# Performance work log

Measured on AMD Instinct MI355X. Metric: run time of the kernel, lower is better.

The kernel has to match this reference:

```python
import jax, jax.numpy as jnp
import numpy as np

N_NODES = 200000
N_EDGES = 800000
C1, E1 = 20000, 80000
C2, E2 = 2000, 8000
N_IN, N_HID, K_BLOCK = 24, 64, 6
N_OUT = 6
BN_EPS = 1e-5


def cheb_conv(x, edge_index, W, b, n):
    """PyG ChebConv with lambda_max=2: L_hat = -D^-1/2 A D^-1/2."""
    src, dst = edge_index[0], edge_index[1]
    K = W.shape[0]
    deg = jax.ops.segment_sum(jnp.ones(src.shape[0], x.dtype), dst, num_segments=n)
    dis = jnp.where(deg > 0, 1.0 / jnp.sqrt(jnp.maximum(deg, 1.0)), 0.0)
    norm = -(dis[src] * dis[dst])[:, None]  # [E,1]

    def prop(h):
        return jax.ops.segment_sum(h[src] * norm, dst, num_segments=n)

    Tx0 = x
    out = Tx0 @ W[0]
    if K > 1:
        Tx1 = prop(Tx0)
        out = out + Tx1 @ W[1]
        for k in range(2, K):
            Tx2 = 2.0 * prop(Tx1) - Tx0
            out = out + Tx2 @ W[k]
            Tx0, Tx1 = Tx1, Tx2
    return out + b


def batchnorm(h, g, bt):
    m = jnp.mean(h, axis=0)
    v = jnp.mean((h - m) ** 2, axis=0)  # biased var, as torch BN forward
    return (h - m) / jnp.sqrt(v + BN_EPS) * g + bt


def kipf_block(x, edge_index, W, b, g, bt, n):
    return jax.nn.relu(batchnorm(cheb_conv(x, edge_index, W, b, n), g, bt))


def segment_mean(x, seg, n_seg):
    s = jax.ops.segment_sum(x, seg, num_segments=n_seg)
    cnt = jax.ops.segment_sum(jnp.ones(x.shape[0], x.dtype), seg, num_segments=n_seg)
    return s / jnp.maximum(cnt, 1.0)[:, None]


def setup_inputs() -> dict:
    key = jax.random.key(0)
    ks = jax.random.split(key, 12)
    inp = {
        "x": jax.random.normal(ks[0], (N_NODES, N_IN), jnp.float32),
        "edge_index": jax.random.randint(ks[1], (2, N_EDGES), 0, N_NODES),
        "cluster1": jax.random.randint(ks[2], (N_NODES,), 0, C1),
        "cluster2": jax.random.randint(ks[3], (N_NODES,), 0, C2),
        "edge_index_c1": jax.random.randint(ks[4], (2, E1), 0, C1),
        "edge_index_c2": jax.random.randint(ks[5], (2, E2), 0, C2),
    }
    sc = 1.0 / np.sqrt(N_IN * K_BLOCK)
    for i, kk in zip((1, 2, 3), (ks[6], ks[7], ks[8])):
        inp[f"W{i}"] = jax.random.normal(kk, (K_BLOCK, N_IN, N_HID), jnp.float32) * sc
        inp[f"b{i}"] = jnp.zeros((N_HID,), jnp.float32)
        inp[f"g{i}"] = jnp.ones((N_HID,), jnp.float32)
        inp[f"bt{i}"] = jnp.zeros((N_HID,), jnp.float32)
    n_mix = 3 * N_HID + N_IN
    inp["Wm"] = jax.random.normal(ks[9], (1, n_mix, N_OUT), jnp.float32) / np.sqrt(n_mix)
    inp["bm"] = jnp.zeros((N_OUT,), jnp.float32)
    return inp


def reference(x, edge_index, cluster1, cluster2, edge_index_c1, edge_index_c2,
              W1, b1, g1, bt1, W2, b2, g2, bt2, W3, b3, g3, bt3, Wm, bm):
    # branch 1: full-resolution graph
    h1 = kipf_block(x, edge_index, W1, b1, g1, bt1, N_NODES)
    # branch 2: cluster1-pooled graph, then unpool
    xp1 = segment_mean(x, cluster1, C1)
    h2 = kipf_block(xp1, edge_index_c1, W2, b2, g2, bt2, C1)[cluster1]
    # branch 3: cluster2-pooled graph, then unpool
    xp2 = segment_mean(x, cluster2, C2)
    h3 = kipf_block(xp2, edge_index_c2, W3, b3, g3, bt3, C2)[cluster2]
    # skip concat with raw input, then mixing conv (K=1 -> identity Cheb term)
    mix = jnp.concatenate([h1, h2, h3, x], axis=1)
    return cheb_conv(mix, edge_index, Wm, bm, N_NODES)
```

## Files before the change

kernel.cpp:

```cpp
#include <hip/hip_runtime.h>
#include <algorithm>

#define FIN 24
#define NHID 64
#define NMIX 216
#define NOUT 6
#define BN_EPS 1e-5f

__global__ void k_hist(const int* __restrict__ ei, int E, int* deg) {
    int e = blockIdx.x * blockDim.x + threadIdx.x;
    if (e < E) atomicAdd(&deg[ei[E + e]], 1);
}

__global__ void k_dis(const int* __restrict__ deg, float* dis, int n) {
    int i = blockIdx.x * blockDim.x + threadIdx.x;
    if (i < n) { int v = deg[i]; dis[i] = v > 0 ? rsqrtf((float)v) : 0.f; }
}

__global__ void k_scan_local(const int* __restrict__ deg, int n, int* rowptr, int* bsum) {
    __shared__ int s[256];
    int i = blockIdx.x * 256 + threadIdx.x;
    int v = (i < n) ? deg[i] : 0;
    s[threadIdx.x] = v;
    __syncthreads();
#pragma unroll
    for (int off = 1; off < 256; off <<= 1) {
        int x = (threadIdx.x >= off) ? s[threadIdx.x - off] : 0;
        __syncthreads();
        s[threadIdx.x] += x;
        __syncthreads();
    }
    if (i <= n) rowptr[i] = s[threadIdx.x] - v;
    if (threadIdx.x == 255) bsum[blockIdx.x] = s[255];
}

__global__ void k_scan_bsum(int* bsum, int nb) {
    __shared__ int s[256];
    int carry = 0;
    for (int base = 0; base < nb; base += 256) {
        int i = base + threadIdx.x;
        int v = (i < nb) ? bsum[i] : 0;
        s[threadIdx.x] = v;
        __syncthreads();
#pragma unroll
        for (int off = 1; off < 256; off <<= 1) {
            int x = (threadIdx.x >= off) ? s[threadIdx.x - off] : 0;
            __syncthreads();
            s[threadIdx.x] += x;
            __syncthreads();
        }
        if (i < nb) bsum[i] = s[threadIdx.x] - v + carry;
        carry += s[255];
        __syncthreads();
    }
}

__global__ void k_scan_add(int* rowptr, const int* __restrict__ bsum, int n) {
    int i = blockIdx.x * 256 + threadIdx.x;
    if (i <= n) rowptr[i] += bsum[blockIdx.x];
}

__global__ void k_fill(const int* __restrict__ ei, int E, const float* __restrict__ dis,
                       const int* __restrict__ rowptr, int* fill,
                       int* __restrict__ col, float* __restrict__ val) {
    int e = blockIdx.x * blockDim.x + threadIdx.x;
    if (e >= E) return;
    int s = ei[e], d = ei[E + e];
    int slot = rowptr[d] + atomicAdd(&fill[d], 1);
    col[slot] = s;
    val[slot] = -dis[s] * dis[d];
}

__global__ void k_propg(const int* __restrict__ rowptr, const int* __restrict__ col,
                        const float* __restrict__ val, float scale,
                        const float* __restrict__ h, const float* __restrict__ prev,
                        float* __restrict__ out, int n) {
    int t = blockIdx.x * blockDim.x + threadIdx.x;
    if (t >= n) return;
    int beg = rowptr[t], end = rowptr[t + 1];
    float4 a[6];
#pragma unroll
    for (int q = 0; q < 6; ++q) a[q] = make_float4(0.f, 0.f, 0.f, 0.f);
    for (int e = beg; e < end; ++e) {
        float w = val[e];
        const float4* hp = reinterpret_cast<const float4*>(h + (size_t)col[e] * FIN);
#pragma unroll
        for (int q = 0; q < 6; ++q) {
            float4 hv = hp[q];
            a[q].x = fmaf(w, hv.x, a[q].x);
            a[q].y = fmaf(w, hv.y, a[q].y);
            a[q].z = fmaf(w, hv.z, a[q].z);
            a[q].w = fmaf(w, hv.w, a[q].w);
        }
    }
    float4* op = reinterpret_cast<float4*>(out + (size_t)t * FIN);
    if (prev) {
        const float4* pp = reinterpret_cast<const float4*>(prev + (size_t)t * FIN);
#pragma unroll
        for (int q = 0; q < 6; ++q) {
            float4 pv = pp[q];
            op[q] = make_float4(fmaf(scale, a[q].x, -pv.x), fmaf(scale, a[q].y, -pv.y),
                                fmaf(scale, a[q].z, -pv.z), fmaf(scale, a[q].w, -pv.w));
        }
    } else {
#pragma unroll
        for (int q = 0; q < 6; ++q)
            op[q] = make_float4(scale * a[q].x, scale * a[q].y, scale * a[q].z, scale * a[q].w);
    }
}

__global__ void k_gemv2(const float* __restrict__ S1, const float* __restrict__ S2,
                        const float* __restrict__ Wa, const float* __restrict__ Wb,
                        const float* __restrict__ bias, float* __restrict__ acc,
                        float* __restrict__ stats, int n) {
    __shared__ float sb[4][2][16 * FIN];
    int j = threadIdx.x & 63;
    int w = threadIdx.x >> 6;
    float wa[FIN], wb[FIN];
#pragma unroll
    for (int f = 0; f < FIN; ++f) wa[f] = Wa[f * NHID + j];
#pragma unroll
    for (int f = 0; f < FIN; ++f) wb[f] = Wb[f * NHID + j];
    int nbase = blockIdx.x * 64 + w * 16;
#pragma unroll
    for (int k = 0; k < 3; ++k) {
        int i = k * 64 + j;
        int half = i / 96;
        int j4 = i - half * 96;
        int nd = j4 / 6, q = j4 - nd * 6;
        int node = nbase + nd;
        const float* src = (half ? S2 : S1) + (size_t)node * FIN + q * 4;
        float4 v = (node < n) ? *reinterpret_cast<const float4*>(src)
                              : make_float4(0.f, 0.f, 0.f, 0.f);
        *reinterpret_cast<float4*>(&sb[w][half][j4 * 4]) = v;
    }
    float sum = 0.f, sq = 0.f;
#pragma unroll 2
    for (int nd = 0; nd < 16; ++nd) {
        int node = nbase + nd;
        bool ok = (node < n);
        int nodec = ok ? node : 0;
        float base = bias ? bias[j] : acc[(size_t)nodec * NHID + j];
        const float4* r1 = reinterpret_cast<const float4*>(&sb[w][0][nd * FIN]);
        const float4* r2 = reinterpret_cast<const float4*>(&sb[w][1][nd * FIN]);
        float a = 0.f, p = 0.f;
#pragma unroll
        for (int t = 0; t < 6; ++t) {
            float4 v = r1[t];
            a = fmaf(v.x, wa[t * 4 + 0], a);
            p = fmaf(v.y, wa[t * 4 + 1], p);
            a = fmaf(v.z, wa[t * 4 + 2], a);
            p = fmaf(v.w, wa[t * 4 + 3], p);
        }
#pragma unroll
        for (int t = 0; t < 6; ++t) {
            float4 v = r2[t];
            a = fmaf(v.x, wb[t * 4 + 0], a);
            p = fmaf(v.y, wb[t * 4 + 1], p);
            a = fmaf(v.z, wb[t * 4 + 2], a);
            p = fmaf(v.w, wb[t * 4 + 3], p);
        }
        float r = base + a + p;
        if (ok) {
            acc[(size_t)node * NHID + j] = r;
            sum += r; sq = fmaf(r, r, sq);
        }
    }
    if (stats) {
        __shared__ float rs[256], rq[256];
        rs[threadIdx.x] = sum; rq[threadIdx.x] = sq;
        __syncthreads();
        if (threadIdx.x < 64) {
            float s = rs[threadIdx.x] + rs[threadIdx.x + 64] + rs[threadIdx.x + 128] + rs[threadIdx.x + 192];
            float q = rq[threadIdx.x] + rq[threadIdx.x + 64] + rq[threadIdx.x + 128] + rq[threadIdx.x + 192];
            atomicAdd(&stats[threadIdx.x], s);
            atomicAdd(&stats[NHID + threadIdx.x], q);
        }
    }
}

__global__ void k_bnprep3(const float* __restrict__ st1, const float* __restrict__ g1,
                          const float* __restrict__ bt1, float inv1,
                          const float* __restrict__ st2, const float* __restrict__ g2,
                          const float* __restrict__ bt2, float inv2,
                          const float* __restrict__ st3, const float* __restrict__ g3,
                          const float* __restrict__ bt3, float inv3,
                          float* __restrict__ s1, float* __restrict__ s2,
                          float* __restrict__ s3) {
    int b = threadIdx.x >> 6, i = threadIdx.x & 63;
    const float* st = (b == 0) ? st1 : (b == 1) ? st2 : st3;
    const float* g  = (b == 0) ? g1  : (b == 1) ? g2  : g3;
    const float* bt = (b == 0) ? bt1 : (b == 1) ? bt2 : bt3;
    float inv       = (b == 0) ? inv1 : (b == 1) ? inv2 : inv3;
    float* so       = (b == 0) ? s1  : (b == 1) ? s2  : s3;
    float m = st[i] * inv;
    float v = st[NHID + i] * inv - m * m;
    float sc = g[i] * rsqrtf(v + BN_EPS);
    so[i] = sc;
    so[NHID + i] = fmaf(-m, sc, bt[i]);
}

__global__ void k_scatter(const float* __restrict__ x, const int* __restrict__ cl,
                          int n, float* xp, float* cnt) {
    int idx = blockIdx.x * blockDim.x + threadIdx.x;
    if (idx >= n * FIN) return;
    int node = idx / FIN, f = idx - node * FIN;
    int c = cl[node];
    atomicAdd(&xp[c * FIN + f], x[idx]);
    if (f == 0) atomicAdd(&cnt[c], 1.f);
}

__global__ void k_divcnt(float* xp, const float* __restrict__ cnt, int c) {
    int idx = blockIdx.x * blockDim.x + threadIdx.x;
    if (idx >= c * FIN) return;
    xp[idx] = xp[idx] / fmaxf(cnt[idx / FIN], 1.f);
}

__global__ void k_final(const float* __restrict__ acc1, const float* __restrict__ sc1,
                        const float* __restrict__ h2, const float* __restrict__ sc2,
                        const int* __restrict__ cl1,
                        const float* __restrict__ h3, const float* __restrict__ sc3,
                        const int* __restrict__ cl2,
                        const float* __restrict__ x, const float* __restrict__ Wm,
                        const float* __restrict__ bm, float* __restrict__ out, int n) {
    int t = blockIdx.x * blockDim.x + threadIdx.x;
    if (t >= n) return;
    float o[NOUT];
#pragma unroll
    for (int j = 0; j < NOUT; ++j) o[j] = bm[j];
    {
        const float4* r4 = reinterpret_cast<const float4*>(acc1 + (size_t)t * NHID);
#pragma unroll
        for (int i4 = 0; i4 < NHID / 4; ++i4) {
            float4 v = r4[i4];
            float hv[4] = {v.x, v.y, v.z, v.w};
#pragma unroll
            for (int c = 0; c < 4; ++c) {
                int i = i4 * 4 + c;
                float h = fmaxf(fmaf(hv[c], sc1[i], sc1[NHID + i]), 0.f);
#pragma unroll
                for (int j = 0; j < NOUT; ++j) o[j] = fmaf(h, Wm[i * NOUT + j], o[j]);
            }
        }
    }
    {
        const float4* r4 = reinterpret_cast<const float4*>(h2 + (size_t)cl1[t] * NHID);
#pragma unroll
        for (int i4 = 0; i4 < NHID / 4; ++i4) {
            float4 v = r4[i4];
            float hv[4] = {v.x, v.y, v.z, v.w};
#pragma unroll
            for (int c = 0; c < 4; ++c) {
                int hid = i4 * 4 + c;
                float h = fmaxf(fmaf(hv[c], sc2[hid], sc2[NHID + hid]), 0.f);
#pragma unroll
                for (int j = 0; j < NOUT; ++j) o[j] = fmaf(h, Wm[(NHID + hid) * NOUT + j], o[j]);
            }
        }
    }
    {
        const float4* r4 = reinterpret_cast<const float4*>(h3 + (size_t)cl2[t] * NHID);
#pragma unroll
        for (int i4 = 0; i4 < NHID / 4; ++i4) {
            float4 v = r4[i4];
            float hv[4] = {v.x, v.y, v.z, v.w};
#pragma unroll
            for (int c = 0; c < 4; ++c) {
                int hid = i4 * 4 + c;
                float h = fmaxf(fmaf(hv[c], sc3[hid], sc3[NHID + hid]), 0.f);
#pragma unroll
                for (int j = 0; j < NOUT; ++j) o[j] = fmaf(h, Wm[(2 * NHID + hid) * NOUT + j], o[j]);
            }
        }
    }
    {
        const float4* r4 = reinterpret_cast<const float4*>(x + (size_t)t * FIN);
#pragma unroll
        for (int i4 = 0; i4 < FIN / 4; ++i4) {
            float4 v = r4[i4];
            float hv[4] = {v.x, v.y, v.z, v.w};
#pragma unroll
            for (int c = 0; c < 4; ++c) {
                int i = 3 * NHID + i4 * 4 + c;
#pragma unroll
                for (int j = 0; j < NOUT; ++j) o[j] = fmaf(hv[c], Wm[i * NOUT + j], o[j]);
            }
        }
    }
    float* op = out + (size_t)t * NOUT;
#pragma unroll
    for (int j = 0; j < NOUT; ++j) op[j] = o[j];
}

extern "C" void kernel_launch(void* const* d_in, const int* in_sizes, int n_in,
                              void* d_out, int out_size, void* d_ws, size_t ws_size,
                              hipStream_t stream) {
    const int N = 200000, E = 800000;
    const int C1n = 20000, E1 = 80000;
    const int C2n = 2000, E2 = 8000;

    const float* x  = (const float*)d_in[0];
    const int* ei   = (const int*)d_in[1];
    const int* cl1  = (const int*)d_in[2];
    const int* cl2  = (const int*)d_in[3];
    const int* eic1 = (const int*)d_in[4];
    const int* eic2 = (const int*)d_in[5];
    const float* W1 = (const float*)d_in[6];  const float* b1 = (const float*)d_in[7];
    const float* g1 = (const float*)d_in[8];  const float* bt1 = (const float*)d_in[9];
    const float* W2 = (const float*)d_in[10]; const float* b2 = (const float*)d_in[11];
    const float* g2 = (const float*)d_in[12]; const float* bt2 = (const float*)d_in[13];
    const float* W3 = (const float*)d_in[14]; const float* b3 = (const float*)d_in[15];
    const float* g3 = (const float*)d_in[16]; const float* bt3 = (const float*)d_in[17];
    const float* Wm = (const float*)d_in[18]; const float* bm = (const float*)d_in[19];

    char* wb = (char*)d_ws;
    size_t off = 0;
    auto alloc = [&](size_t nwords) {
        void* p = wb + off; off += ((nwords + 3) & ~(size_t)3) * 4; return p;
    };
    int* degi1 = (int*)alloc(N);   int* fill1 = (int*)alloc(N);
    int* degi2 = (int*)alloc(C1n); int* fill2 = (int*)alloc(C1n);
    int* degi3 = (int*)alloc(C2n); int* fill3 = (int*)alloc(C2n);
    float* st1 = (float*)alloc(128); float* st2 = (float*)alloc(128); float* st3 = (float*)alloc(128);
    float* xp1 = (float*)alloc((size_t)C1n * FIN); float* cnt1 = (float*)alloc(C1n);
    float* xp2 = (float*)alloc((size_t)C2n * FIN); float* cnt2 = (float*)alloc(C2n);
    size_t zero_bytes = off;
    int* rp1 = (int*)alloc(N + 1);   int* col1 = (int*)alloc(E);  float* val1 = (float*)alloc(E);
    int* rp2 = (int*)alloc(C1n + 1); int* col2 = (int*)alloc(E1); float* val2 = (float*)alloc(E1);
    int* rp3 = (int*)alloc(C2n + 1); int* col3 = (int*)alloc(E2); float* val3 = (float*)alloc(E2);
    float* dis1 = (float*)alloc(N); float* dis2 = (float*)alloc(C1n); float* dis3 = (float*)alloc(C2n);
    int* bsum = (int*)alloc(1024);
    float* scsh1 = (float*)alloc(128); float* scsh2 = (float*)alloc(128); float* scsh3 = (float*)alloc(128);
    float* B1_0 = (float*)alloc((size_t)N * FIN);   float* B1_1 = (float*)alloc((size_t)N * FIN);
    float* B2_0 = (float*)alloc((size_t)C1n * FIN); float* B2_1 = (float*)alloc((size_t)C1n * FIN);
    float* B3_0 = (float*)alloc((size_t)C2n * FIN); float* B3_1 = (float*)alloc((size_t)C2n * FIN);
    float* acc1 = (float*)alloc((size_t)N * NHID);
    float* acc2 = (float*)alloc((size_t)C1n * NHID);
    float* acc3 = (float*)alloc((size_t)C2n * NHID);
    if (off > ws_size) return;

    hipMemsetAsync(d_ws, 0, zero_bytes, stream);

    const int T = 256;
    auto cdiv = [](int a, int b) { return (a + b - 1) / b; };

    auto branch = [&](const float* xin, int n, const int* e, int Ecnt,
                      const float* W, const float* bb, int* degi, int* fill, float* dis,
                      int* rp, int* col, float* val,
                      float* B0, float* Bb1, float* acc, float* st) {
        int ge = cdiv(Ecnt, T), gn = cdiv(n, T);
        int nb = cdiv(n + 1, 256);
        int gg = cdiv(n, 64);
        const int WSZ = FIN * NHID;
        k_hist<<<ge, T, 0, stream>>>(e, Ecnt, degi);
        k_dis<<<gn, T, 0, stream>>>(degi, dis, n);
        k_scan_local<<<nb, 256, 0, stream>>>(degi, n, rp, bsum);
        k_scan_bsum<<<1, 256, 0, stream>>>(bsum, nb);
        k_scan_add<<<nb, 256, 0, stream>>>(rp, bsum, n);
        k_fill<<<ge, T, 0, stream>>>(e, Ecnt, dis, rp, fill, col, val);
        k_propg<<<gn, T, 0, stream>>>(rp, col, val, 1.0f, xin, nullptr, B0, n);
        k_gemv2<<<gg, T, 0, stream>>>(xin, B0, W, W + WSZ, bb, acc, nullptr, n);
        k_propg<<<gn, T, 0, stream>>>(rp, col, val, 2.0f, B0, xin, Bb1, n);
        k_propg<<<gn, T, 0, stream>>>(rp, col, val, 2.0f, Bb1, B0, B0, n);
        k_gemv2<<<gg, T, 0, stream>>>(Bb1, B0, W + 2 * WSZ, W + 3 * WSZ, nullptr, acc, nullptr, n);
        k_propg<<<gn, T, 0, stream>>>(rp, col, val, 2.0f, B0, Bb1, Bb1, n);
        k_propg<<<gn, T, 0, stream>>>(rp, col, val, 2.0f, Bb1, B0, B0, n);
        k_gemv2<<<gg, T, 0, stream>>>(Bb1, B0, W + 4 * WSZ, W + 5 * WSZ, nullptr, acc, st, n);
    };

    branch(x, N, ei, E, W1, b1, degi1, fill1, dis1, rp1, col1, val1, B1_0, B1_1, acc1, st1);
    k_scatter<<<cdiv(N * FIN, T), T, 0, stream>>>(x, cl1, N, xp1, cnt1);
    k_divcnt<<<cdiv(C1n * FIN, T), T, 0, stream>>>(xp1, cnt1, C1n);
    branch(xp1, C1n, eic1, E1, W2, b2, degi2, fill2, dis2, rp2, col2, val2, B2_0, B2_1, acc2, st2);
    k_scatter<<<cdiv(N * FIN, T), T, 0, stream>>>(x, cl2, N, xp2, cnt2);
    k_divcnt<<<cdiv(C2n * FIN, T), T, 0, stream>>>(xp2, cnt2, C2n);
    branch(xp2, C2n, eic2, E2, W3, b3, degi3, fill3, dis3, rp3, col3, val3, B3_0, B3_1, acc3, st3);
    k_bnprep3<<<1, 192, 0, stream>>>(st1, g1, bt1, 1.0f / (float)N,
                                     st2, g2, bt2, 1.0f / (float)C1n,
                                     st3, g3, bt3, 1.0f / (float)C2n,
                                     scsh1, scsh2, scsh3);
    k_final<<<cdiv(N, T), T, 0, stream>>>(acc1, scsh1, acc2, scsh2, cl1,
                                          acc3, scsh3, cl2,
                                          x, Wm, bm, (float*)d_out, N);
}
```

Baseline: 760.8 us.

## Split SpMM propagation across six threads per node and pack CSR col/val

The propagation kernel now assigns one float4 feature chunk per thread, six threads per node, so neighbor-row gathers are coalesced across lanes. Edges are unrolled by two with dual accumulators. The CSR column and weight arrays are packed into one int2 array so each edge needs a single load. The gemv kernel preloads the 16 base values per thread before the loop and fully unrolls it, at the cost of more registers. Each thread now re-reads rowptr and the edge list redundantly, six times per node.

Measured after the change: 679.6 us. 10.7% less time.

```diff
diff --git a/kernel.cpp b/kernel.cpp
--- a/kernel.cpp
+++ b/kernel.cpp
@@ -61,52 +61,52 @@
 }
 
 __global__ void k_fill(const int* __restrict__ ei, int E, const float* __restrict__ dis,
-                       const int* __restrict__ rowptr, int* fill,
-                       int* __restrict__ col, float* __restrict__ val) {
+                       const int* __restrict__ rowptr, int* fill, int2* __restrict__ cv) {
     int e = blockIdx.x * blockDim.x + threadIdx.x;
     if (e >= E) return;
     int s = ei[e], d = ei[E + e];
     int slot = rowptr[d] + atomicAdd(&fill[d], 1);
-    col[slot] = s;
-    val[slot] = -dis[s] * dis[d];
-}
-
-__global__ void k_propg(const int* __restrict__ rowptr, const int* __restrict__ col,
-                        const float* __restrict__ val, float scale,
-                        const float* __restrict__ h, const float* __restrict__ prev,
-                        float* __restrict__ out, int n) {
-    int t = blockIdx.x * blockDim.x + threadIdx.x;
-    if (t >= n) return;
-    int beg = rowptr[t], end = rowptr[t + 1];
-    float4 a[6];
-#pragma unroll
-    for (int q = 0; q < 6; ++q) a[q] = make_float4(0.f, 0.f, 0.f, 0.f);
-    for (int e = beg; e < end; ++e) {
-        float w = val[e];
-        const float4* hp = reinterpret_cast<const float4*>(h + (size_t)col[e] * FIN);
-#pragma unroll
-        for (int q = 0; q < 6; ++q) {
-            float4 hv = hp[q];
-            a[q].x = fmaf(w, hv.x, a[q].x);
-            a[q].y = fmaf(w, hv.y, a[q].y);
-            a[q].z = fmaf(w, hv.z, a[q].z);
-            a[q].w = fmaf(w, hv.w, a[q].w);
-        }
-    }
-    float4* op = reinterpret_cast<float4*>(out + (size_t)t * FIN);
+    cv[slot] = make_int2(s, __float_as_int(-dis[s] * dis[d]));
+}
+
+__global__ void k_propg(const int* __restrict__ rowptr, const int2* __restrict__ cv,
+                        float scale, const float* __restrict__ h,
+                        const float* __restrict__ prev, float* __restrict__ out, int n) {
+    int idx = blockIdx.x * blockDim.x + threadIdx.x;
+    if (idx >= n * 6) return;
+    int d = idx / 6, q = idx - d * 6;
+    int beg = rowptr[d], end = rowptr[d + 1];
+    const float4* h4 = reinterpret_cast<const float4*>(h);
+    float ax = 0.f, ay = 0.f, az = 0.f, aw = 0.f;
+    float bx = 0.f, by = 0.f, bz = 0.f, bw = 0.f;
+    int e = beg;
+    for (; e + 2 <= end; e += 2) {
+        int2 c0 = cv[e], c1 = cv[e + 1];
+        float w0 = __int_as_float(c0.y), w1 = __int_as_float(c1.y);
+        float4 h0 = h4[(size_t)c0.x * 6 + q];
+        float4 h1 = h4[(size_t)c1.x * 6 + q];
+        ax = fmaf(w0, h0.x, ax); ay = fmaf(w0, h0.y, ay);
+        az = fmaf(w0, h0.z, az); aw = fmaf(w0, h0.w, aw);
+        bx = fmaf(w1, h1.x, bx); by = fmaf(w1, h1.y, by);
+        bz = fmaf(w1, h1.z, bz); bw = fmaf(w1, h1.w, bw);
+    }
+    if (e < end) {
+        int2 c0 = cv[e];
+        float w0 = __int_as_float(c0.y);
+        float4 h0 = h4[(size_t)c0.x * 6 + q];
+        ax = fmaf(w0, h0.x, ax); ay = fmaf(w0, h0.y, ay);
+        az = fmaf(w0, h0.z, az); aw = fmaf(w0, h0.w, aw);
+    }
+    ax += bx; ay += by; az += bz; aw += bw;
+    float4 r;
     if (prev) {
-        const float4* pp = reinterpret_cast<const float4*>(prev + (size_t)t * FIN);
-#pragma unroll
-        for (int q = 0; q < 6; ++q) {
-            float4 pv = pp[q];
-            op[q] = make_float4(fmaf(scale, a[q].x, -pv.x), fmaf(scale, a[q].y, -pv.y),
-                                fmaf(scale, a[q].z, -pv.z), fmaf(scale, a[q].w, -pv.w));
-        }
+        float4 pv = reinterpret_cast<const float4*>(prev)[idx];
+        r = make_float4(fmaf(scale, ax, -pv.x), fmaf(scale, ay, -pv.y),
+                        fmaf(scale, az, -pv.z), fmaf(scale, aw, -pv.w));
     } else {
-#pragma unroll
-        for (int q = 0; q < 6; ++q)
-            op[q] = make_float4(scale * a[q].x, scale * a[q].y, scale * a[q].z, scale * a[q].w);
-    }
+        r = make_float4(scale * ax, scale * ay, scale * az, scale * aw);
+    }
+    reinterpret_cast<float4*>(out)[idx] = r;
 }
 
 __global__ void k_gemv2(const float* __restrict__ S1, const float* __restrict__ S2,
@@ -116,12 +116,24 @@
     __shared__ float sb[4][2][16 * FIN];
     int j = threadIdx.x & 63;
     int w = threadIdx.x >> 6;
+    int nbase = blockIdx.x * 64 + w * 16;
+    float bases[16];
+    if (bias) {
+        float bb = bias[j];
+#pragma unroll
+        for (int nd = 0; nd < 16; ++nd) bases[nd] = bb;
+    } else {
+#pragma unroll
+        for (int nd = 0; nd < 16; ++nd) {
+            int node = nbase + nd;
+            bases[nd] = (node < n) ? acc[(size_t)node * NHID + j] : 0.f;
+        }
+    }
     float wa[FIN], wb[FIN];
 #pragma unroll
     for (int f = 0; f < FIN; ++f) wa[f] = Wa[f * NHID + j];
 #pragma unroll
     for (int f = 0; f < FIN; ++f) wb[f] = Wb[f * NHID + j];
-    int nbase = blockIdx.x * 64 + w * 16;
 #pragma unroll
     for (int k = 0; k < 3; ++k) {
         int i = k * 64 + j;
@@ -135,12 +147,9 @@
         *reinterpret_cast<float4*>(&sb[w][half][j4 * 4]) = v;
     }
     float sum = 0.f, sq = 0.f;
-#pragma unroll 2
+#pragma unroll
     for (int nd = 0; nd < 16; ++nd) {
         int node = nbase + nd;
-        bool ok = (node < n);
-        int nodec = ok ? node : 0;
-        float base = bias ? bias[j] : acc[(size_t)nodec * NHID + j];
         const float4* r1 = reinterpret_cast<const float4*>(&sb[w][0][nd * FIN]);
         const float4* r2 = reinterpret_cast<const float4*>(&sb[w][1][nd * FIN]);
         float a = 0.f, p = 0.f;
@@ -160,8 +169,8 @@
             a = fmaf(v.z, wb[t * 4 + 2], a);
             p = fmaf(v.w, wb[t * 4 + 3], p);
         }
-        float r = base + a + p;
-        if (ok) {
+        float r = bases[nd] + a + p;
+        if (node < n) {
             acc[(size_t)node * NHID + j] = r;
             sum += r; sq = fmaf(r, r, sq);
         }
@@ -325,9 +334,9 @@
     float* xp1 = (float*)alloc((size_t)C1n * FIN); float* cnt1 = (float*)alloc(C1n);
     float* xp2 = (float*)alloc((size_t)C2n * FIN); float* cnt2 = (float*)alloc(C2n);
     size_t zero_bytes = off;
-    int* rp1 = (int*)alloc(N + 1);   int* col1 = (int*)alloc(E);  float* val1 = (float*)alloc(E);
-    int* rp2 = (int*)alloc(C1n + 1); int* col2 = (int*)alloc(E1); float* val2 = (float*)alloc(E1);
-    int* rp3 = (int*)alloc(C2n + 1); int* col3 = (int*)alloc(E2); float* val3 = (float*)alloc(E2);
+    int* rp1 = (int*)alloc(N + 1);   int2* cv1 = (int2*)alloc(2 * (size_t)E);
+    int* rp2 = (int*)alloc(C1n + 1); int2* cv2 = (int2*)alloc(2 * (size_t)E1);
+    int* rp3 = (int*)alloc(C2n + 1); int2* cv3 = (int2*)alloc(2 * (size_t)E2);
     float* dis1 = (float*)alloc(N); float* dis2 = (float*)alloc(C1n); float* dis3 = (float*)alloc(C2n);
     int* bsum = (int*)alloc(1024);
     float* scsh1 = (float*)alloc(128); float* scsh2 = (float*)alloc(128); float* scsh3 = (float*)alloc(128);
@@ -346,35 +355,35 @@
 
     auto branch = [&](const float* xin, int n, const int* e, int Ecnt,
                       const float* W, const float* bb, int* degi, int* fill, float* dis,
-                      int* rp, int* col, float* val,
-                      float* B0, float* Bb1, float* acc, float* st) {
+                      int* rp, int2* cv, float* B0, float* Bb1, float* acc, float* st) {
         int ge = cdiv(Ecnt, T), gn = cdiv(n, T);
         int nb = cdiv(n + 1, 256);
         int gg = cdiv(n, 64);
+        int gp = cdiv(n * 6, T);
         const int WSZ = FIN * NHID;
         k_hist<<<ge, T, 0, stream>>>(e, Ecnt, degi);
         k_dis<<<gn, T, 0, stream>>>(degi, dis, n);
         k_scan_local<<<nb, 256, 0, stream>>>(degi, n, rp, bsum);
         k_scan_bsum<<<1, 256, 0, stream>>>(bsum, nb);
         k_scan_add<<<nb, 256, 0, stream>>>(rp, bsum, n);
-        k_fill<<<ge, T, 0, stream>>>(e, Ecnt, dis, rp, fill, col, val);
-        k_propg<<<gn, T, 0, stream>>>(rp, col, val, 1.0f, xin, nullptr, B0, n);
+        k_fill<<<ge, T, 0, stream>>>(e, Ecnt, dis, rp, fill, cv);
+        k_propg<<<gp, T, 0, stream>>>(rp, cv, 1.0f, xin, nullptr, B0, n);
         k_gemv2<<<gg, T, 0, stream>>>(xin, B0, W, W + WSZ, bb, acc, nullptr, n);
-        k_propg<<<gn, T, 0, stream>>>(rp, col, val, 2.0f, B0, xin, Bb1, n);
-        k_propg<<<gn, T, 0, stream>>>(rp, col, val, 2.0f, Bb1, B0, B0, n);
+        k_propg<<<gp, T, 0, stream>>>(rp, cv, 2.0f, B0, xin, Bb1, n);
+        k_propg<<<gp, T, 0, stream>>>(rp, cv, 2.0f, Bb1, B0, B0, n);
         k_gemv2<<<gg, T, 0, stream>>>(Bb1, B0, W + 2 * WSZ, W + 3 * WSZ, nullptr, acc, nullptr, n);
-        k_propg<<<gn, T, 0, stream>>>(rp, col, val, 2.0f, B0, Bb1, Bb1, n);
-        k_propg<<<gn, T, 0, stream>>>(rp, col, val, 2.0f, Bb1, B0, B0, n);
+        k_propg<<<gp, T, 0, stream>>>(rp, cv, 2.0f, B0, Bb1, Bb1, n);
+        k_propg<<<gp, T, 0, stream>>>(rp, cv, 2.0f, Bb1, B0, B0, n);
         k_gemv2<<<gg, T, 0, stream>>>(Bb1, B0, W + 4 * WSZ, W + 5 * WSZ, nullptr, acc, st, n);
     };
 
-    branch(x, N, ei, E, W1, b1, degi1, fill1, dis1, rp1, col1, val1, B1_0, B1_1, acc1, st1);
+    branch(x, N, ei, E, W1, b1, degi1, fill1, dis1, rp1, cv1, B1_0, B1_1, acc1, st1);
     k_scatter<<<cdiv(N * FIN, T), T, 0, stream>>>(x, cl1, N, xp1, cnt1);
     k_divcnt<<<cdiv(C1n * FIN, T), T, 0, stream>>>(xp1, cnt1, C1n);
-    branch(xp1, C1n, eic1, E1, W2, b2, degi2, fill2, dis2, rp2, col2, val2, B2_0, B2_1, acc2, st2);
+    branch(xp1, C1n, eic1, E1, W2, b2, degi2, fill2, dis2, rp2, cv2, B2_0, B2_1, acc2, st2);
     k_scatter<<<cdiv(N * FIN, T), T, 0, stream>>>(x, cl2, N, xp2, cnt2);
     k_divcnt<<<cdiv(C2n * FIN, T), T, 0, stream>>>(xp2, cnt2, C2n);
-    branch(xp2, C2n, eic2, E2, W3, b3, degi3, fill3, dis3, rp3, col3, val3, B3_0, B3_1, acc3, st3);
+    branch(xp2, C2n, eic2, E2, W3, b3, degi3, fill3, dis3, rp3, cv3, B3_0, B3_1, acc3, st3);
     k_bnprep3<<<1, 192, 0, stream>>>(st1, g1, bt1, 1.0f / (float)N,
                                      st2, g2, bt2, 1.0f / (float)C1n,
                                      st3, g3, bt3, 1.0f / (float)C2n,
```
